# Kernel optimization log

Hardware: AMD Instinct MI355X
Metric: run time of the kernel (lower is better)

The kernel has to match this reference:

```python
import jax, jax.numpy as jnp
import numpy as np

RADIUS = 0.25
NUM_NEIGHBORS = 32
POS_DIM = 24
STEM_C = 64
PATCH_C = 256
LN_EPS = 1e-5


def query_ball_point(radius, nsample, xyz, new_xyz):
    # xyz: [B,N,3], new_xyz: [B,S,3] -> idx [B,S,nsample] (PointNet++ ball query)
    N = xyz.shape[1]
    sqr = (jnp.sum(new_xyz ** 2, -1)[:, :, None]
           + jnp.sum(xyz ** 2, -1)[:, None, :]
           - 2.0 * jnp.einsum('bsd,bnd->bsn', new_xyz, xyz))  # [B,S,N]
    idx = jnp.broadcast_to(jnp.arange(N, dtype=jnp.int32), sqr.shape)
    idx = jnp.where(sqr > radius * radius, N, idx)
    idx = jnp.sort(idx, axis=-1)[..., :nsample]  # first nsample in-ball (by index order)
    first = idx[..., :1]
    idx = jnp.where(idx == N, first, idx)  # pad empty slots with first neighbor
    return idx


def index_points(points, idx):
    # points [B,N,C], idx [B,S,K] -> [B,S,K,C]
    return jax.vmap(lambda p, i: p[i])(points, idx)


def rel_pos_encoding(rel_xyz, dim=POS_DIM):
    # sinusoidal Fourier encoding of 3D offsets: 3 coords * 2 (sin,cos) * dim//6 freqs
    nf = dim // 6
    freqs = 2.0 ** jnp.arange(nf, dtype=rel_xyz.dtype)
    ang = rel_xyz[..., None] * freqs  # [...,3,nf]
    enc = jnp.concatenate([jnp.sin(ang), jnp.cos(ang)], axis=-1)  # [...,3,2nf]
    return enc.reshape(rel_xyz.shape[:-1] + (dim,))


def point_mlp(x, W, b, gamma, beta, activate):
    h = jnp.einsum('...i,io->...o', x, W) + b
    mu = jnp.mean(h, -1, keepdims=True)
    var = jnp.mean((h - mu) ** 2, -1, keepdims=True)
    h = (h - mu) * jax.lax.rsqrt(var + LN_EPS) * gamma + beta
    return jax.nn.gelu(h, approximate=False) if activate else h


def setup_inputs() -> dict:
    key = jax.random.key(0)
    ks = jax.random.split(key, 8)
    B, N, S = 8, 16384, 1024
    in_c = STEM_C + 3 + POS_DIM  # 91
    return {
        'xyz': jax.random.uniform(ks[0], (B, N, 3), dtype=jnp.float32),
        'point_feature': jax.random.normal(ks[1], (B, N, STEM_C), dtype=jnp.float32),
        'patch_center': jax.random.uniform(ks[2], (B, S, 3), dtype=jnp.float32),
        'W1': jax.random.normal(ks[3], (in_c, PATCH_C), dtype=jnp.float32) * 0.02,
        'b1': jnp.zeros((PATCH_C,), jnp.float32),
        'g1': jnp.ones((PATCH_C,), jnp.float32),
        'be1': jnp.zeros((PATCH_C,), jnp.float32),
        'W2': jax.random.normal(ks[4], (PATCH_C, PATCH_C), dtype=jnp.float32) * 0.02,
        'b2': jnp.zeros((PATCH_C,), jnp.float32),
        'g2': jnp.ones((PATCH_C,), jnp.float32),
        'be2': jnp.zeros((PATCH_C,), jnp.float32),
    }


def reference(xyz, point_feature, patch_center, W1, b1, g1, be1, W2, b2, g2, be2):
    neighbor_idx = query_ball_point(RADIUS, NUM_NEIGHBORS, xyz, patch_center)  # [B,S,K]
    grouped_xyz = index_points(xyz, neighbor_idx)              # [B,S,K,3]
    grouped_feature = index_points(point_feature, neighbor_idx)  # [B,S,K,C]
    relative_xyz = grouped_xyz - patch_center[:, :, None, :]
    relative_position = rel_pos_encoding(relative_xyz)         # [B,S,K,24]
    grouped_input = jnp.concatenate((grouped_feature, relative_xyz, relative_position), axis=-1)
    h = point_mlp(grouped_input, W1, b1, g1, be1, True)
    h = point_mlp(h, W2, b2, g2, be2, False)
    patch_feature = jnp.max(h, axis=2)                         # max over neighbors -> [B,S,PATCH_C]
    return patch_feature, neighbor_idx
```

## Files before the change

kernel.cpp:

```cpp
#include <hip/hip_runtime.h>
#include <math.h>

#define NPTS 16384
#define KN 32
#define C 256
#define NQ 8192
#define PF_ELEMS (NQ * C)

#define W1P_ELEMS (3 * 16 * 64 * 8)
#define W2P_ELEMS (8 * 16 * 64 * 8)
#define HSTR 264

typedef _Float16 half8 __attribute__((ext_vector_type(8)));
typedef _Float16 half4v __attribute__((ext_vector_type(4)));
typedef float f32x4 __attribute__((ext_vector_type(4)));

__global__ void prep_w_kernel(const float* __restrict__ W1,
                              const float* __restrict__ W2,
                              _Float16* __restrict__ wp) {
    const int e = blockIdx.x * 256 + threadIdx.x;
    if (e < W1P_ELEMS) {
        const int j = e & 7, lane = (e >> 3) & 63, nt = (e >> 9) & 15, kt = e >> 13;
        const int k = kt * 32 + (lane >> 4) * 8 + j;
        const int n = nt * 16 + (lane & 15);
        wp[e] = (_Float16)((k < 91) ? W1[k * C + n] : 0.0f);
    } else {
        const int e2 = e - W1P_ELEMS;
        const int j = e2 & 7, lane = (e2 >> 3) & 63, nt = (e2 >> 9) & 15, kt = e2 >> 13;
        const int k = kt * 32 + (lane >> 4) * 8 + j;
        const int n = nt * 16 + (lane & 15);
        wp[e] = (_Float16)W2[k * C + n];
    }
}

__device__ __forceinline__ float gelu_tanh(float x) {
    const float t  = x * x;
    const float p2 = fmaf(t, 0.0713548162726f, 1.59576912161f);
    const float e  = __expf(x * p2);
    return x - x * __builtin_amdgcn_rcpf(e + 1.0f);
}

__global__ void __launch_bounds__(256, 5)
encoder_fused(const float* __restrict__ xyz,
              const float* __restrict__ pf,
              const float* __restrict__ ctr,
              const float* __restrict__ b1, const float* __restrict__ g1,
              const float* __restrict__ be1,
              const float* __restrict__ b2, const float* __restrict__ g2,
              const float* __restrict__ be2,
              const _Float16* __restrict__ w1p,
              const _Float16* __restrict__ w2p,
              float* __restrict__ out0,
              float* __restrict__ out1) {
    const int q = blockIdx.x;
    const int b = q >> 10;
    const int t = threadIdx.x;
    const int w = t >> 6;
    const int lane = t & 63;
    const int quad = lane >> 4;
    const int l15  = lane & 15;

    __shared__ __align__(16) unsigned char H16raw[KN * HSTR * 2];
    __shared__ __align__(16) unsigned char Xsraw[KN * 104 * 2];
    __shared__ float lnp[4 * 256];
    __shared__ __align__(16) float sums[KN][12];
    __shared__ int nbr[KN];
    __shared__ int wcnt[2][4];

    _Float16 (*H16)[HSTR] = (_Float16(*)[HSTR])H16raw;
    _Float16 (*Xs)[104]   = (_Float16(*)[104])Xsraw;
    float* lng1  = lnp;        float* lnbe1 = lnp + 256;
    float* lng2  = lnp + 512;  float* lnbe2 = lnp + 768;

    lnp[t]       = g1[t];  lnp[256 + t] = be1[t];
    lnp[512 + t] = g2[t];  lnp[768 + t] = be2[t];

    const float* xb = xyz + (size_t)b * NPTS * 3;
    const float cx = ctr[q * 3 + 0];
    const float cy = ctr[q * 3 + 1];
    const float cz = ctr[q * 3 + 2];
    const float sc = __fadd_rn(__fadd_rn(__fmul_rn(cx, cx), __fmul_rn(cy, cy)),
                               __fmul_rn(cz, cz));

    int found = 0;
    int par = 0;
    for (int base = 0; base < NPTS; base += 256) {
        const int n = base + t;
        const float px = xb[n * 3 + 0];
        const float py = xb[n * 3 + 1];
        const float pz = xb[n * 3 + 2];
        const float sp = __fadd_rn(__fadd_rn(__fmul_rn(px, px), __fmul_rn(py, py)),
                                   __fmul_rn(pz, pz));
        const float dt = __fadd_rn(__fadd_rn(__fmul_rn(cx, px), __fmul_rn(cy, py)),
                                   __fmul_rn(cz, pz));
        const float sqr = __fsub_rn(__fadd_rn(sc, sp), __fmul_rn(2.0f, dt));
        const bool inball = (sqr <= 0.0625f);

        const unsigned long long m = __ballot(inball);
        if (lane == 0) wcnt[par][w] = (int)__popcll(m);
        __syncthreads();
        int pre = found;
        if (w > 0) pre += wcnt[par][0];
        if (w > 1) pre += wcnt[par][1];
        if (w > 2) pre += wcnt[par][2];
        const int tot = found + wcnt[par][0] + wcnt[par][1] + wcnt[par][2] + wcnt[par][3];
        const int pos = pre + (int)__popcll(m & ((1ull << lane) - 1ull));
        if (inball && pos < KN) nbr[pos] = n;
        found = tot;
        par ^= 1;
        if (found >= KN) break;
    }
    __syncthreads();
    const int count = (found < KN) ? found : KN;
    const int first = (count > 0) ? nbr[0] : NPTS;

    if (t < KN)
        out1[(size_t)q * KN + t] = (float)((t < count) ? nbr[t] : first);

    {
        const int k  = t >> 3;
        const int tc = t & 7;
        const int nidx = (k < count) ? nbr[k] : first;
        const int n = (nidx < NPTS) ? nidx : NPTS - 1;
        const float rx = xb[n * 3 + 0] - cx;
        const float ry = xb[n * 3 + 1] - cy;
        const float rz = xb[n * 3 + 2] - cz;
        const float* pfr = pf + ((size_t)b * NPTS + n) * 64;

        const float4 f0 = *(const float4*)(pfr + tc * 8);
        const float4 f1 = *(const float4*)(pfr + tc * 8 + 4);
        half8 hv;
        hv[0] = (_Float16)f0.x; hv[1] = (_Float16)f0.y;
        hv[2] = (_Float16)f0.z; hv[3] = (_Float16)f0.w;
        hv[4] = (_Float16)f1.x; hv[5] = (_Float16)f1.y;
        hv[6] = (_Float16)f1.z; hv[7] = (_Float16)f1.w;
        *(half8*)&Xs[k][tc * 8] = hv;

        half4v ov;
        #pragma unroll
        for (int j = 0; j < 4; ++j) {
            const int c = 64 + tc * 4 + j;
            float v;
            if (c < 67) {
                v = (c == 64) ? rx : ((c == 65) ? ry : rz);
            } else if (c < 91) {
                const int jj = c - 67;
                const int d = jj >> 3;
                const int mm = jj & 7;
                const float f = (float)(1 << (mm & 3));
                const float r = (d == 0) ? rx : ((d == 1) ? ry : rz);
                v = (mm < 4) ? __sinf(r * f) : __cosf(r * f);
            } else {
                v = 0.0f;
            }
            ov[j] = (_Float16)v;
        }
        *(half4v*)&Xs[k][64 + tc * 4] = ov;
    }
    __syncthreads();

    const int qx = (quad ^ (l15 >> 2)) * 8;

    f32x4 acc[2][4];

    #pragma unroll
    for (int mt = 0; mt < 2; ++mt)
        #pragma unroll
        for (int nt = 0; nt < 4; ++nt)
            acc[mt][nt] = (f32x4){0.f, 0.f, 0.f, 0.f};

    #pragma unroll
    for (int kt = 0; kt < 3; ++kt) {
        const half8 a0 = *(const half8*)&Xs[l15][kt * 32 + quad * 8];
        const half8 a1 = *(const half8*)&Xs[16 + l15][kt * 32 + quad * 8];
        #pragma unroll
        for (int nt = 0; nt < 4; ++nt) {
            const int ntg = w * 4 + nt;
            const half8 bf = *(const half8*)&w1p[((kt * 16 + ntg) * 64 + lane) * 8];
            acc[0][nt] = __builtin_amdgcn_mfma_f32_16x16x32_f16(a0, bf, acc[0][nt], 0, 0, 0);
            acc[1][nt] = __builtin_amdgcn_mfma_f32_16x16x32_f16(a1, bf, acc[1][nt], 0, 0, 0);
        }
    }

    {
        #pragma unroll
        for (int nt = 0; nt < 4; ++nt) {
            const float bb = b1[w * 64 + nt * 16 + l15];
            #pragma unroll
            for (int mt = 0; mt < 2; ++mt)
                #pragma unroll
                for (int r = 0; r < 4; ++r)
                    acc[mt][nt][r] += bb;
        }
        float s[2][4], z[2][4];
        #pragma unroll
        for (int mt = 0; mt < 2; ++mt)
            #pragma unroll
            for (int r = 0; r < 4; ++r) {
                const float a = acc[mt][0][r], bb = acc[mt][1][r];
                const float c = acc[mt][2][r], d = acc[mt][3][r];
                s[mt][r] = (a + bb) + (c + d);
                z[mt][r] = fmaf(a, a, fmaf(bb, bb, fmaf(c, c, d * d)));
            }
        #pragma unroll
        for (int off = 1; off < 16; off <<= 1) {
            #pragma unroll
            for (int mt = 0; mt < 2; ++mt)
                #pragma unroll
                for (int r = 0; r < 4; ++r) {
                    s[mt][r] += __shfl_xor(s[mt][r], off, 64);
                    z[mt][r] += __shfl_xor(z[mt][r], off, 64);
                }
        }
        if (l15 == 0) {
            #pragma unroll
            for (int mt = 0; mt < 2; ++mt)
                #pragma unroll
                for (int r = 0; r < 4; ++r) {
                    const int row = 16 * mt + 4 * quad + r;
                    float2 v; v.x = s[mt][r]; v.y = z[mt][r];
                    *(float2*)&sums[row][2 * w] = v;
                }
        }
        __syncthreads();
        float mu[2][4], rs[2][4];
        #pragma unroll
        for (int mt = 0; mt < 2; ++mt)
            #pragma unroll
            for (int r = 0; r < 4; ++r) {
                const int row = 16 * mt + 4 * quad + r;
                const f32x4 v0 = *(const f32x4*)&sums[row][0];
                const f32x4 v1 = *(const f32x4*)&sums[row][4];
                const float ss = (v0.x + v0.z) + (v1.x + v1.z);
                const float qq = (v0.y + v0.w) + (v1.y + v1.w);
                const float m  = ss * (1.0f / 256.0f);
                const float va = fmaf(qq, 1.0f / 256.0f, -m * m);
                mu[mt][r] = m;
                rs[mt][r] = __builtin_amdgcn_rsqf(va + 1e-5f);
            }
        #pragma unroll
        for (int nt = 0; nt < 4; ++nt) {
            const int col  = w * 64 + nt * 16 + l15;
            const int colp = col ^ (quad << 3);
            const float g  = lng1[col];
            const float be = lnbe1[col];
            #pragma unroll
            for (int mt = 0; mt < 2; ++mt)
                #pragma unroll
                for (int r = 0; r < 4; ++r) {
                    const float y = fmaf((acc[mt][nt][r] - mu[mt][r]) * rs[mt][r], g, be);
                    H16[16 * mt + 4 * quad + r][colp] = (_Float16)gelu_tanh(y);
                }
        }
    }
    __syncthreads();

    #pragma unroll
    for (int mt = 0; mt < 2; ++mt)
        #pragma unroll
        for (int nt = 0; nt < 4; ++nt)
            acc[mt][nt] = (f32x4){0.f, 0.f, 0.f, 0.f};

    #pragma unroll
    for (int kt = 0; kt < 8; ++kt) {
        const half8 a0 = *(const half8*)&H16[l15][kt * 32 + qx];
        const half8 a1 = *(const half8*)&H16[16 + l15][kt * 32 + qx];
        #pragma unroll
        for (int nt = 0; nt < 4; ++nt) {
            const int ntg = w * 4 + nt;
            const half8 bf = *(const half8*)&w2p[((kt * 16 + ntg) * 64 + lane) * 8];
            acc[0][nt] = __builtin_amdgcn_mfma_f32_16x16x32_f16(a0, bf, acc[0][nt], 0, 0, 0);
            acc[1][nt] = __builtin_amdgcn_mfma_f32_16x16x32_f16(a1, bf, acc[1][nt], 0, 0, 0);
        }
    }

    {
        #pragma unroll
        for (int nt = 0; nt < 4; ++nt) {
            const float bb = b2[w * 64 + nt * 16 + l15];
            #pragma unroll
            for (int mt = 0; mt < 2; ++mt)
                #pragma unroll
                for (int r = 0; r < 4; ++r)
                    acc[mt][nt][r] += bb;
        }
        float s[2][4], z[2][4];
        #pragma unroll
        for (int mt = 0; mt < 2; ++mt)
            #pragma unroll
            for (int r = 0; r < 4; ++r) {
                const float a = acc[mt][0][r], bb = acc[mt][1][r];
                const float c = acc[mt][2][r], d = acc[mt][3][r];
                s[mt][r] = (a + bb) + (c + d);
                z[mt][r] = fmaf(a, a, fmaf(bb, bb, fmaf(c, c, d * d)));
            }
        #pragma unroll
        for (int off = 1; off < 16; off <<= 1) {
            #pragma unroll
            for (int mt = 0; mt < 2; ++mt)
                #pragma unroll
                for (int r = 0; r < 4; ++r) {
                    s[mt][r] += __shfl_xor(s[mt][r], off, 64);
                    z[mt][r] += __shfl_xor(z[mt][r], off, 64);
                }
        }
        if (l15 == 0) {
            #pragma unroll
            for (int mt = 0; mt < 2; ++mt)
                #pragma unroll
                for (int r = 0; r < 4; ++r) {
                    const int row = 16 * mt + 4 * quad + r;
                    float2 v; v.x = s[mt][r]; v.y = z[mt][r];
                    *(float2*)&sums[row][2 * w] = v;
                }
        }
        __syncthreads();
        float mu[2][4], rs[2][4];
        #pragma unroll
        for (int mt = 0; mt < 2; ++mt)
            #pragma unroll
            for (int r = 0; r < 4; ++r) {
                const int row = 16 * mt + 4 * quad + r;
                const f32x4 v0 = *(const f32x4*)&sums[row][0];
                const f32x4 v1 = *(const f32x4*)&sums[row][4];
                const float ss = (v0.x + v0.z) + (v1.x + v1.z);
                const float qq = (v0.y + v0.w) + (v1.y + v1.w);
                const float m  = ss * (1.0f / 256.0f);
                const float va = fmaf(qq, 1.0f / 256.0f, -m * m);
                mu[mt][r] = m;
                rs[mt][r] = __builtin_amdgcn_rsqf(va + 1e-5f);
            }
        #pragma unroll
        for (int nt = 0; nt < 4; ++nt) {
            const int col  = w * 64 + nt * 16 + l15;
            const float g  = lng2[col];
            const float be = lnbe2[col];
            float mx = -INFINITY;
            #pragma unroll
            for (int mt = 0; mt < 2; ++mt)
                #pragma unroll
                for (int r = 0; r < 4; ++r) {
                    const float y = fmaf((acc[mt][nt][r] - mu[mt][r]) * rs[mt][r], g, be);
                    mx = fmaxf(mx, y);
                }
            mx = fmaxf(mx, __shfl_xor(mx, 16, 64));
            mx = fmaxf(mx, __shfl_xor(mx, 32, 64));
            if (quad == 0)
                out0[(size_t)q * C + col] = mx;
        }
    }
}

extern "C" void kernel_launch(void* const* d_in, const int* in_sizes, int n_in,
                              void* d_out, int out_size, void* d_ws, size_t ws_size,
                              hipStream_t stream) {
    const float* xyz = (const float*)d_in[0];
    const float* pf  = (const float*)d_in[1];
    const float* ctr = (const float*)d_in[2];
    const float* W1  = (const float*)d_in[3];
    const float* b1  = (const float*)d_in[4];
    const float* g1  = (const float*)d_in[5];
    const float* be1 = (const float*)d_in[6];
    const float* W2  = (const float*)d_in[7];
    const float* b2  = (const float*)d_in[8];
    const float* g2  = (const float*)d_in[9];
    const float* be2 = (const float*)d_in[10];

    float* out = (float*)d_out;
    _Float16* wp = (_Float16*)d_ws;

    prep_w_kernel<<<(W1P_ELEMS + W2P_ELEMS) / 256, 256, 0, stream>>>(W1, W2, wp);
    encoder_fused<<<NQ, 256, 0, stream>>>(xyz, pf, ctr,
                                          b1, g1, be1, b2, g2, be2,
                                          wp, wp + W1P_ELEMS,
                                          out, out + PF_ELEMS);
}
```

Measured before the change: 212.8 us.

## Swap MFMA operand order to make outputs row-per-lane and fold bias into GEMM

Swaps the MFMA A/B operands so each lane holds four consecutive channels of one neighbor row. This replaces the 16-lane shuffle reductions for the LayerNorm statistics with two cross-quad shuffles and allows vectorized half4 stores to H16 and f32x4 loads of gamma/beta. The first-layer bias is folded into the GEMM as a constant-one input column (k=91), and the shared-memory copy of the LayerNorm parameters is dropped so the kernel can target occupancy 6. The final max-over-neighbors reduction now runs a 16-lane shuffle, and outputs are written as float4. Reading gamma/beta from global memory and relying on the MFMA layout flip are the main correctness and perf risks.

```diff
diff --git a/kernel.cpp b/kernel.cpp
--- a/kernel.cpp
+++ b/kernel.cpp
@@ -14,24 +14,6 @@
 typedef _Float16 half8 __attribute__((ext_vector_type(8)));
 typedef _Float16 half4v __attribute__((ext_vector_type(4)));
 typedef float f32x4 __attribute__((ext_vector_type(4)));
-
-__global__ void prep_w_kernel(const float* __restrict__ W1,
-                              const float* __restrict__ W2,
-                              _Float16* __restrict__ wp) {
-    const int e = blockIdx.x * 256 + threadIdx.x;
-    if (e < W1P_ELEMS) {
-        const int j = e & 7, lane = (e >> 3) & 63, nt = (e >> 9) & 15, kt = e >> 13;
-        const int k = kt * 32 + (lane >> 4) * 8 + j;
-        const int n = nt * 16 + (lane & 15);
-        wp[e] = (_Float16)((k < 91) ? W1[k * C + n] : 0.0f);
-    } else {
-        const int e2 = e - W1P_ELEMS;
-        const int j = e2 & 7, lane = (e2 >> 3) & 63, nt = (e2 >> 9) & 15, kt = e2 >> 13;
-        const int k = kt * 32 + (lane >> 4) * 8 + j;
-        const int n = nt * 16 + (lane & 15);
-        wp[e] = (_Float16)W2[k * C + n];
-    }
-}
 
 __device__ __forceinline__ float gelu_tanh(float x) {
     const float t  = x * x;
@@ -40,12 +22,32 @@
     return x - x * __builtin_amdgcn_rcpf(e + 1.0f);
 }
 
-__global__ void __launch_bounds__(256, 5)
+__global__ void prep_w_kernel(const float* __restrict__ W1,
+                              const float* __restrict__ b1,
+                              const float* __restrict__ W2,
+                              _Float16* __restrict__ wp) {
+    const int idx = blockIdx.x * 256 + threadIdx.x;
+    if (idx < 96 * 256) {
+        const int k = idx >> 8, n = idx & 255;
+        const float v = (k < 91) ? W1[k * 256 + n] : ((k == 91) ? b1[n] : 0.0f);
+        const int kt = k >> 5, quad = (k >> 3) & 3, j = k & 7;
+        const int nt = n >> 4, l15 = n & 15;
+        wp[(((kt * 16 + nt) * 64) + quad * 16 + l15) * 8 + j] = (_Float16)v;
+    } else {
+        const int e = idx - 96 * 256;
+        const int k = e >> 8, n = e & 255;
+        const int kt = k >> 5, quad = (k >> 3) & 3, j = k & 7;
+        const int nt = n >> 4, l15 = n & 15;
+        wp[W1P_ELEMS + (((kt * 16 + nt) * 64) + quad * 16 + l15) * 8 + j] =
+            (_Float16)W2[k * 256 + n];
+    }
+}
+
+__global__ void __launch_bounds__(256, 6)
 encoder_fused(const float* __restrict__ xyz,
               const float* __restrict__ pf,
               const float* __restrict__ ctr,
-              const float* __restrict__ b1, const float* __restrict__ g1,
-              const float* __restrict__ be1,
+              const float* __restrict__ g1, const float* __restrict__ be1,
               const float* __restrict__ b2, const float* __restrict__ g2,
               const float* __restrict__ be2,
               const _Float16* __restrict__ w1p,
@@ -62,18 +64,12 @@
 
     __shared__ __align__(16) unsigned char H16raw[KN * HSTR * 2];
     __shared__ __align__(16) unsigned char Xsraw[KN * 104 * 2];
-    __shared__ float lnp[4 * 256];
-    __shared__ __align__(16) float sums[KN][12];
+    __shared__ float sums[KN][10];
     __shared__ int nbr[KN];
     __shared__ int wcnt[2][4];
 
     _Float16 (*H16)[HSTR] = (_Float16(*)[HSTR])H16raw;
     _Float16 (*Xs)[104]   = (_Float16(*)[104])Xsraw;
-    float* lng1  = lnp;        float* lnbe1 = lnp + 256;
-    float* lng2  = lnp + 512;  float* lnbe2 = lnp + 768;
-
-    lnp[t]       = g1[t];  lnp[256 + t] = be1[t];
-    lnp[512 + t] = g2[t];  lnp[768 + t] = be2[t];
 
     const float* xb = xyz + (size_t)b * NPTS * 3;
     const float cx = ctr[q * 3 + 0];
@@ -150,6 +146,8 @@
                 const float f = (float)(1 << (mm & 3));
                 const float r = (d == 0) ? rx : ((d == 1) ? ry : rz);
                 v = (mm < 4) ? __sinf(r * f) : __cosf(r * f);
+            } else if (c == 91) {
+                v = 1.0f;
             } else {
                 v = 0.0f;
             }
@@ -159,8 +157,6 @@
     }
     __syncthreads();
 
-    const int qx = (quad ^ (l15 >> 2)) * 8;
-
     f32x4 acc[2][4];
 
     #pragma unroll
@@ -171,86 +167,65 @@
 
     #pragma unroll
     for (int kt = 0; kt < 3; ++kt) {
-        const half8 a0 = *(const half8*)&Xs[l15][kt * 32 + quad * 8];
-        const half8 a1 = *(const half8*)&Xs[16 + l15][kt * 32 + quad * 8];
-        #pragma unroll
-        for (int nt = 0; nt < 4; ++nt) {
-            const int ntg = w * 4 + nt;
-            const half8 bf = *(const half8*)&w1p[((kt * 16 + ntg) * 64 + lane) * 8];
-            acc[0][nt] = __builtin_amdgcn_mfma_f32_16x16x32_f16(a0, bf, acc[0][nt], 0, 0, 0);
-            acc[1][nt] = __builtin_amdgcn_mfma_f32_16x16x32_f16(a1, bf, acc[1][nt], 0, 0, 0);
+        const half8 x0 = *(const half8*)&Xs[l15][kt * 32 + quad * 8];
+        const half8 x1 = *(const half8*)&Xs[16 + l15][kt * 32 + quad * 8];
+        #pragma unroll
+        for (int nt = 0; nt < 4; ++nt) {
+            const half8 wf = *(const half8*)&w1p[((kt * 16 + w * 4 + nt) * 64 + lane) * 8];
+            acc[0][nt] = __builtin_amdgcn_mfma_f32_16x16x32_f16(wf, x0, acc[0][nt], 0, 0, 0);
+            acc[1][nt] = __builtin_amdgcn_mfma_f32_16x16x32_f16(wf, x1, acc[1][nt], 0, 0, 0);
         }
     }
 
     {
-        #pragma unroll
-        for (int nt = 0; nt < 4; ++nt) {
-            const float bb = b1[w * 64 + nt * 16 + l15];
-            #pragma unroll
-            for (int mt = 0; mt < 2; ++mt)
-                #pragma unroll
-                for (int r = 0; r < 4; ++r)
-                    acc[mt][nt][r] += bb;
-        }
-        float s[2][4], z[2][4];
-        #pragma unroll
-        for (int mt = 0; mt < 2; ++mt)
+        float s0 = 0.f, z0 = 0.f, s1 = 0.f, z1 = 0.f;
+        #pragma unroll
+        for (int nt = 0; nt < 4; ++nt)
             #pragma unroll
             for (int r = 0; r < 4; ++r) {
-                const float a = acc[mt][0][r], bb = acc[mt][1][r];
-                const float c = acc[mt][2][r], d = acc[mt][3][r];
-                s[mt][r] = (a + bb) + (c + d);
-                z[mt][r] = fmaf(a, a, fmaf(bb, bb, fmaf(c, c, d * d)));
-            }
-        #pragma unroll
-        for (int off = 1; off < 16; off <<= 1) {
-            #pragma unroll
-            for (int mt = 0; mt < 2; ++mt)
-                #pragma unroll
-                for (int r = 0; r < 4; ++r) {
-                    s[mt][r] += __shfl_xor(s[mt][r], off, 64);
-                    z[mt][r] += __shfl_xor(z[mt][r], off, 64);
-                }
-        }
-        if (l15 == 0) {
-            #pragma unroll
-            for (int mt = 0; mt < 2; ++mt)
-                #pragma unroll
-                for (int r = 0; r < 4; ++r) {
-                    const int row = 16 * mt + 4 * quad + r;
-                    float2 v; v.x = s[mt][r]; v.y = z[mt][r];
-                    *(float2*)&sums[row][2 * w] = v;
-                }
+                const float a0 = acc[0][nt][r], a1 = acc[1][nt][r];
+                s0 += a0; z0 = fmaf(a0, a0, z0);
+                s1 += a1; z1 = fmaf(a1, a1, z1);
+            }
+        s0 += __shfl_xor(s0, 16, 64); s0 += __shfl_xor(s0, 32, 64);
+        z0 += __shfl_xor(z0, 16, 64); z0 += __shfl_xor(z0, 32, 64);
+        s1 += __shfl_xor(s1, 16, 64); s1 += __shfl_xor(s1, 32, 64);
+        z1 += __shfl_xor(z1, 16, 64); z1 += __shfl_xor(z1, 32, 64);
+        if (quad == 0) {
+            float2 v0; v0.x = s0; v0.y = z0;
+            float2 v1; v1.x = s1; v1.y = z1;
+            *(float2*)&sums[l15][2 * w]      = v0;
+            *(float2*)&sums[16 + l15][2 * w] = v1;
         }
         __syncthreads();
-        float mu[2][4], rs[2][4];
-        #pragma unroll
-        for (int mt = 0; mt < 2; ++mt)
+        float st0 = 0.f, zt0 = 0.f, st1 = 0.f, zt1 = 0.f;
+        #pragma unroll
+        for (int ww = 0; ww < 4; ++ww) {
+            const float2 v0 = *(const float2*)&sums[l15][2 * ww];
+            const float2 v1 = *(const float2*)&sums[16 + l15][2 * ww];
+            st0 += v0.x; zt0 += v0.y;
+            st1 += v1.x; zt1 += v1.y;
+        }
+        const float mu0 = st0 * (1.0f / 256.0f);
+        const float mu1 = st1 * (1.0f / 256.0f);
+        const float rs0 = __builtin_amdgcn_rsqf(fmaf(zt0, 1.0f / 256.0f, -mu0 * mu0) + 1e-5f);
+        const float rs1 = __builtin_amdgcn_rsqf(fmaf(zt1, 1.0f / 256.0f, -mu1 * mu1) + 1e-5f);
+
+        #pragma unroll
+        for (int nt = 0; nt < 4; ++nt) {
+            const int chb = (w * 4 + nt) * 16 + quad * 4;
+            const f32x4 g  = *(const f32x4*)&g1[chb];
+            const f32x4 be = *(const f32x4*)&be1[chb];
+            half4v h0, h1;
             #pragma unroll
             for (int r = 0; r < 4; ++r) {
-                const int row = 16 * mt + 4 * quad + r;
-                const f32x4 v0 = *(const f32x4*)&sums[row][0];
-                const f32x4 v1 = *(const f32x4*)&sums[row][4];
-                const float ss = (v0.x + v0.z) + (v1.x + v1.z);
-                const float qq = (v0.y + v0.w) + (v1.y + v1.w);
-                const float m  = ss * (1.0f / 256.0f);
-                const float va = fmaf(qq, 1.0f / 256.0f, -m * m);
-                mu[mt][r] = m;
-                rs[mt][r] = __builtin_amdgcn_rsqf(va + 1e-5f);
-            }
-        #pragma unroll
-        for (int nt = 0; nt < 4; ++nt) {
-            const int col  = w * 64 + nt * 16 + l15;
-            const int colp = col ^ (quad << 3);
-            const float g  = lng1[col];
-            const float be = lnbe1[col];
-            #pragma unroll
-            for (int mt = 0; mt < 2; ++mt)
-                #pragma unroll
-                for (int r = 0; r < 4; ++r) {
-                    const float y = fmaf((acc[mt][nt][r] - mu[mt][r]) * rs[mt][r], g, be);
-                    H16[16 * mt + 4 * quad + r][colp] = (_Float16)gelu_tanh(y);
-                }
+                const float y0 = fmaf((acc[0][nt][r] - mu0) * rs0, g[r], be[r]);
+                const float y1 = fmaf((acc[1][nt][r] - mu1) * rs1, g[r], be[r]);
+                h0[r] = (_Float16)gelu_tanh(y0);
+                h1[r] = (_Float16)gelu_tanh(y1);
+            }
+            *(half4v*)&H16[l15][chb]      = h0;
+            *(half4v*)&H16[16 + l15][chb] = h1;
         }
     }
     __syncthreads();
@@ -263,90 +238,91 @@
 
     #pragma unroll
     for (int kt = 0; kt < 8; ++kt) {
-        const half8 a0 = *(const half8*)&H16[l15][kt * 32 + qx];
-        const half8 a1 = *(const half8*)&H16[16 + l15][kt * 32 + qx];
-        #pragma unroll
-        for (int nt = 0; nt < 4; ++nt) {
-            const int ntg = w * 4 + nt;
-            const half8 bf = *(const half8*)&w2p[((kt * 16 + ntg) * 64 + lane) * 8];
-            acc[0][nt] = __builtin_amdgcn_mfma_f32_16x16x32_f16(a0, bf, acc[0][nt], 0, 0, 0);
-            acc[1][nt] = __builtin_amdgcn_mfma_f32_16x16x32_f16(a1, bf, acc[1][nt], 0, 0, 0);
+        const half8 h0 = *(const half8*)&H16[l15][kt * 32 + quad * 8];
+        const half8 h1 = *(const half8*)&H16[16 + l15][kt * 32 + quad * 8];
+        #pragma unroll
+        for (int nt = 0; nt < 4; ++nt) {
+            const half8 wf = *(const half8*)&w2p[((kt * 16 + w * 4 + nt) * 64 + lane) * 8];
+            acc[0][nt] = __builtin_amdgcn_mfma_f32_16x16x32_f16(wf, h0, acc[0][nt], 0, 0, 0);
+            acc[1][nt] = __builtin_amdgcn_mfma_f32_16x16x32_f16(wf, h1, acc[1][nt], 0, 0, 0);
         }
     }
 
     {
         #pragma unroll
         for (int nt = 0; nt < 4; ++nt) {
-            const float bb = b2[w * 64 + nt * 16 + l15];
-            #pragma unroll
-            for (int mt = 0; mt < 2; ++mt)
-                #pragma unroll
-                for (int r = 0; r < 4; ++r)
-                    acc[mt][nt][r] += bb;
-        }
-        float s[2][4], z[2][4];
-        #pragma unroll
-        for (int mt = 0; mt < 2; ++mt)
+            const int chb = (w * 4 + nt) * 16 + quad * 4;
+            const f32x4 bv = *(const f32x4*)&b2[chb];
             #pragma unroll
             for (int r = 0; r < 4; ++r) {
-                const float a = acc[mt][0][r], bb = acc[mt][1][r];
-                const float c = acc[mt][2][r], d = acc[mt][3][r];
-                s[mt][r] = (a + bb) + (c + d);
-                z[mt][r] = fmaf(a, a, fmaf(bb, bb, fmaf(c, c, d * d)));
-            }
-        #pragma unroll
-        for (int off = 1; off < 16; off <<= 1) {
-            #pragma unroll
-            for (int mt = 0; mt < 2; ++mt)
-                #pragma unroll
-                for (int r = 0; r < 4; ++r) {
-                    s[mt][r] += __shfl_xor(s[mt][r], off, 64);
-                    z[mt][r] += __shfl_xor(z[mt][r], off, 64);
-                }
-        }
-        if (l15 == 0) {
-            #pragma unroll
-            for (int mt = 0; mt < 2; ++mt)
-                #pragma unroll
-                for (int r = 0; r < 4; ++r) {
-                    const int row = 16 * mt + 4 * quad + r;
-                    float2 v; v.x = s[mt][r]; v.y = z[mt][r];
-                    *(float2*)&sums[row][2 * w] = v;
-                }
+                acc[0][nt][r] += bv[r];
+                acc[1][nt][r] += bv[r];
+            }
+        }
+        float s0 = 0.f, z0 = 0.f, s1 = 0.f, z1 = 0.f;
+        #pragma unroll
+        for (int nt = 0; nt < 4; ++nt)
+            #pragma unroll
+            for (int r = 0; r < 4; ++r) {
+                const float a0 = acc[0][nt][r], a1 = acc[1][nt][r];
+                s0 += a0; z0 = fmaf(a0, a0, z0);
+                s1 += a1; z1 = fmaf(a1, a1, z1);
+            }
+        s0 += __shfl_xor(s0, 16, 64); s0 += __shfl_xor(s0, 32, 64);
+        z0 += __shfl_xor(z0, 16, 64); z0 += __shfl_xor(z0, 32, 64);
+        s1 += __shfl_xor(s1, 16, 64); s1 += __shfl_xor(s1, 32, 64);
+        z1 += __shfl_xor(z1, 16, 64); z1 += __shfl_xor(z1, 32, 64);
+        if (quad == 0) {
+            float2 v0; v0.x = s0; v0.y = z0;
+            float2 v1; v1.x = s1; v1.y = z1;
+            *(float2*)&sums[l15][2 * w]      = v0;
+            *(float2*)&sums[16 + l15][2 * w] = v1;
         }
         __syncthreads();
-        float mu[2][4], rs[2][4];
-        #pragma unroll
-        for (int mt = 0; mt < 2; ++mt)
-            #pragma unroll
-            for (int r = 0; r < 4; ++r) {
-                const int row = 16 * mt + 4 * quad + r;
-                const f32x4 v0 = *(const f32x4*)&sums[row][0];
-                const f32x4 v1 = *(const f32x4*)&sums[row][4];
-                const float ss = (v0.x + v0.z) + (v1.x + v1.z);
-                const float qq = (v0.y + v0.w) + (v1.y + v1.w);
-                const float m  = ss * (1.0f / 256.0f);
-                const float va = fmaf(qq, 1.0f / 256.0f, -m * m);
-                mu[mt][r] = m;
-                rs[mt][r] = __builtin_amdgcn_rsqf(va + 1e-5f);
-            }
-        #pragma unroll
-        for (int nt = 0; nt < 4; ++nt) {
-            const int col  = w * 64 + nt * 16 + l15;
-            const float g  = lng2[col];
-            const float be = lnbe2[col];
-            float mx = -INFINITY;
-            #pragma unroll
-            for (int mt = 0; mt < 2; ++mt)
-                #pragma unroll
-                for (int r = 0; r < 4; ++r) {
-                    const float y = fmaf((acc[mt][nt][r] - mu[mt][r]) * rs[mt][r], g, be);
-                    mx = fmaxf(mx, y);
-                }
-            mx = fmaxf(mx, __shfl_xor(mx, 16, 64));
-            mx = fmaxf(mx, __shfl_xor(mx, 32, 64));
-            if (quad == 0)
-                out0[(size_t)q * C + col] = mx;
+        float st0 = 0.f, zt0 = 0.f, st1 = 0.f, zt1 = 0.f;
+        #pragma unroll
+        for (int ww = 0; ww < 4; ++ww) {
+            const float2 v0 = *(const float2*)&sums[l15][2 * ww];
+            const float2 v1 = *(const float2*)&sums[16 + l15][2 * ww];
+            st0 += v0.x; zt0 += v0.y;
+            st1 += v1.x; zt1 += v1.y;
+        }
+        const float mu0 = st0 * (1.0f / 256.0f);
+        const float mu1 = st1 * (1.0f / 256.0f);
+        const float rs0 = __builtin_amdgcn_rsqf(fmaf(zt0, 1.0f / 256.0f, -mu0 * mu0) + 1e-5f);
+        const float rs1 = __builtin_amdgcn_rsqf(fmaf(zt1, 1.0f / 256.0f, -mu1 * mu1) + 1e-5f);
+
+        #pragma unroll
+        for (int nt = 0; nt < 4; ++nt) {
+            const int chb = (w * 4 + nt) * 16 + quad * 4;
+            const f32x4 g  = *(const f32x4*)&g2[chb];
+            const f32x4 be = *(const f32x4*)&be2[chb];
+            float m0, m1, m2, m3;
+            {
+                const float y00 = fmaf((acc[0][nt][0] - mu0) * rs0, g[0], be[0]);
+                const float y10 = fmaf((acc[1][nt][0] - mu1) * rs1, g[0], be[0]);
+                m0 = fmaxf(y00, y10);
+                const float y01 = fmaf((acc[0][nt][1] - mu0) * rs0, g[1], be[1]);
+                const float y11 = fmaf((acc[1][nt][1] - mu1) * rs1, g[1], be[1]);
+                m1 = fmaxf(y01, y11);
+                const float y02 = fmaf((acc[0][nt][2] - mu0) * rs0, g[2], be[2]);
+                const float y12 = fmaf((acc[1][nt][2] - mu1) * rs1, g[2], be[2]);
+                m2 = fmaxf(y02, y12);
+                const float y03 = fmaf((acc[0][nt][3] - mu0) * rs0, g[3], be[3]);
+                const float y13 = fmaf((acc[1][nt][3] - mu1) * rs1, g[3], be[3]);
+                m3 = fmaxf(y03, y13);
+            }
+            #pragma unroll
+            for (int off = 1; off < 16; off <<= 1) {
+                m0 = fmaxf(m0, __shfl_xor(m0, off, 64));
+                m1 = fmaxf(m1, __shfl_xor(m1, off, 64));
+                m2 = fmaxf(m2, __shfl_xor(m2, off, 64));
+                m3 = fmaxf(m3, __shfl_xor(m3, off, 64));
+            }
+            if (l15 == 0) {
+                f32x4 o; o[0] = m0; o[1] = m1; o[2] = m2; o[3] = m3;
+                *(f32x4*)&out0[(size_t)q * C + chb] = o;
+            }
         }
     }
 }
@@ -369,9 +345,9 @@
     float* out = (float*)d_out;
     _Float16* wp = (_Float16*)d_ws;
 
-    prep_w_kernel<<<(W1P_ELEMS + W2P_ELEMS) / 256, 256, 0, stream>>>(W1, W2, wp);
+    prep_w_kernel<<<(96 * 256 + 65536) / 256, 256, 0, stream>>>(W1, b1, W2, wp);
     encoder_fused<<<NQ, 256, 0, stream>>>(xyz, pf, ctr,
-                                          b1, g1, be1, b2, g2, be2,
+                                          g1, be1, b2, g2, be2,
                                           wp, wp + W1P_ELEMS,
                                           out, out + PF_ELEMS);
 }
```

After: 199.0 us. -6.5%, faster.
